# Kernel optimization log

Measured on AMD Instinct MI355X. Metric: run time of the kernel, lower is better.

Reference implementation:

```python
import jax, jax.numpy as jnp
import numpy as np

HEADS = 16  # module init arg `heads`


def setup_inputs() -> dict:
    key = jax.random.key(0)
    k1, k2, k3 = jax.random.split(key, 3)
    B, T, D = 2, 2048, 1024
    x = jax.random.normal(k1, (B, T, D), dtype=jnp.float32)
    w_qkv = jax.random.normal(k2, (D, 3 * D), dtype=jnp.float32) * (1.0 / np.sqrt(D))
    w_proj = jax.random.normal(k3, (D, D), dtype=jnp.float32) * (1.0 / np.sqrt(D))
    b_proj = jnp.zeros((D,), dtype=jnp.float32)
    return {"x": x, "w_qkv": w_qkv, "w_proj": w_proj, "b_proj": b_proj,
            "window": 16, "stride": 16}


def reference(x, w_qkv, w_proj, b_proj, window, stride):
    B, T, D = x.shape
    H = HEADS
    hd = D // H
    scale = 1.0 / np.sqrt(hd)

    qkv = x @ w_qkv                              # [B,T,3D]
    qkv = qkv.reshape(B, T, 3, H, hd)
    q = jnp.transpose(qkv[:, :, 0], (0, 2, 1, 3))  # [B,H,T,hd]
    k = jnp.transpose(qkv[:, :, 1], (0, 2, 1, 3))
    v = jnp.transpose(qkv[:, :, 2], (0, 2, 1, 3))

    # Local window attention: pad front with zeros (matches F.pad), gather
    # sliding windows so patches[..., t, w, :] = k_padded[..., t + w, :].
    pad = window - 1
    k_pad = jnp.pad(k, ((0, 0), (0, 0), (pad, 0), (0, 0)))
    v_pad = jnp.pad(v, ((0, 0), (0, 0), (pad, 0), (0, 0)))
    win_idx = jnp.arange(T)[:, None] + jnp.arange(window)[None, :]  # [T,W]
    pk = k_pad[:, :, win_idx]                    # [B,H,T,W,hd]
    pv = v_pad[:, :, win_idx]                    # [B,H,T,W,hd]

    attn_local = jnp.einsum('bhtd,bhtwd->bhtw', q, pk) * scale
    attn_local = jax.nn.softmax(attn_local, axis=-1)  # zero-pad keys included, as in torch
    out_local = jnp.einsum('bhtw,bhtwd->bhtd', attn_local, pv)

    # Strided global attention
    g_idx = jnp.arange(0, T, stride)
    kg = k[:, :, g_idx]                          # [B,H,G,hd]
    vg = v[:, :, g_idx]
    attn_g = jnp.einsum('bhtd,bhgd->bhtg', q, kg) * scale
    attn_g = jax.nn.softmax(attn_g, axis=-1)
    out_global = jnp.einsum('bhtg,bhgd->bhtd', attn_g, vg)

    out = out_local + out_global                 # [B,H,T,hd]
    out = jnp.transpose(out, (0, 2, 1, 3)).reshape(B, T, D)
    return out @ w_proj + b_proj
```

## Files before the change

### kernel.cpp

```cpp
#include <hip/hip_runtime.h>
#include <hip/hip_bf16.h>

#define BB 2
#define TT 2048
#define DD 1024
#define HH 16
#define HD 64
#define WIN 16
#define NG 128
#define QKVLD 3072

typedef __bf16 bf16x8 __attribute__((ext_vector_type(8)));
typedef _Float16 f16x8 __attribute__((ext_vector_type(8)));
typedef float f32x4 __attribute__((ext_vector_type(4)));
typedef _Float16 h2 __attribute__((ext_vector_type(2)));

__device__ __forceinline__ unsigned short f2bf(float f) {
    union { float f; unsigned int i; } x; x.f = f;
    unsigned int r = x.i + 0x7FFFu + ((x.i >> 16) & 1u);
    return (unsigned short)(r >> 16);
}
__device__ __forceinline__ unsigned short f2h(float f) {
    union { _Float16 h; unsigned short u; } x; x.h = (_Float16)f; return x.u;
}

__device__ __forceinline__ void gll16(const unsigned short* g, unsigned short* l) {
    __builtin_amdgcn_global_load_lds(
        (const __attribute__((address_space(1))) void*)g,
        (__attribute__((address_space(3))) void*)l,
        16, 0, 0);
}

__global__ __launch_bounds__(256) void prepass_kernel(
    const float* __restrict__ x,
    const float* __restrict__ w_qkv,
    const float* __restrict__ w_proj,
    unsigned short* __restrict__ xb,
    unsigned short* __restrict__ wqkvT,
    unsigned short* __restrict__ wprojT)
{
    __shared__ float tile[64][65];
    const int bid = blockIdx.x;
    const int tid = threadIdx.x;

    if (bid < 2048) {
        const size_t i = ((size_t)bid * 256 + tid) * 8;
        float4 f0 = *(const float4*)(x + i);
        float4 f1 = *(const float4*)(x + i + 4);
        ushort4 a = { f2bf(f0.x), f2bf(f0.y), f2bf(f0.z), f2bf(f0.w) };
        ushort4 b = { f2bf(f1.x), f2bf(f1.y), f2bf(f1.z), f2bf(f1.w) };
        *(ushort4*)(xb + i) = a;
        *(ushort4*)(xb + i + 4) = b;
        return;
    }

    const float* w;
    unsigned short* wT;
    int nblk, kblk, N;
    if (bid < 2816) {
        const int b2 = bid - 2048;
        w = w_qkv; wT = wqkvT; N = 3072;
        nblk = b2 % 48; kblk = b2 / 48;
    } else {
        const int b2 = bid - 2816;
        w = w_proj; wT = wprojT; N = 1024;
        nblk = b2 % 16; kblk = b2 / 16;
    }
    const int K = 1024;
    const int n0 = nblk * 64, k0 = kblk * 64;

    {
        const int krow = tid >> 2;
        const int nc0  = (tid & 3) * 16;
        const float* src = w + (size_t)(k0 + krow) * N + n0 + nc0;
        float4 f0 = *(const float4*)(src);
        float4 f1 = *(const float4*)(src + 4);
        float4 f2 = *(const float4*)(src + 8);
        float4 f3 = *(const float4*)(src + 12);
        *(float4*)&tile[krow][nc0]      = f0;
        *(float4*)&tile[krow][nc0 + 4]  = f1;
        *(float4*)&tile[krow][nc0 + 8]  = f2;
        *(float4*)&tile[krow][nc0 + 12] = f3;
    }
    __syncthreads();
    #pragma unroll
    for (int rep = 0; rep < 2; ++rep) {
        const int n   = (tid >> 3) + rep * 32;
        const int kc0 = (tid & 7) * 8;
        union { uint4 v; unsigned short u[8]; } o;
        #pragma unroll
        for (int j = 0; j < 8; ++j) o.u[j] = f2bf(tile[kc0 + j][n]);
        *(uint4*)(wT + (size_t)(n0 + n) * K + k0 + kc0) = o.v;
    }
}

template<int MODE, int TN>
__global__ __launch_bounds__(256) void gemm_kernel(
    const unsigned short* __restrict__ A,
    const unsigned short* __restrict__ Bt,
    void* __restrict__ Cp,
    const float* __restrict__ bias,
    int M, int N, int K)
{
    constexpr int NJ = TN / 32;
    constexpr int BR = TN / 4;
    __shared__ __align__(16) unsigned short As[128 * 32];
    __shared__ __align__(16) unsigned short Bs[TN * 32];
    const int tid  = threadIdx.x;
    const int wave = tid >> 6;
    const int lane = tid & 63;
    const int lm   = lane & 15;
    const int quad = lane >> 4;
    const int wm   = (wave >> 1) * 64;
    const int wn   = (wave & 1) * (TN / 2);
    const int bm   = blockIdx.y * 128;
    const int bn   = blockIdx.x * TN;

    f32x4 acc[4][NJ];
    const f32x4 z4 = { 0.f, 0.f, 0.f, 0.f };
    #pragma unroll
    for (int i = 0; i < 4; ++i)
        #pragma unroll
        for (int j = 0; j < NJ; ++j) acc[i][j] = z4;

    const int lrow = lane >> 2, lcol = (lane & 3) * 8;
    const unsigned short* gA0 = A  + (size_t)(bm + wave * 32 + lrow) * K + lcol;
    const unsigned short* gA1 = gA0 + (size_t)16 * K;
    const unsigned short* gB0 = Bt + (size_t)(bn + wave * BR + lrow) * K + lcol;
    const unsigned short* gB1 = gB0 + (size_t)16 * K;
    unsigned short* lA0 = &As[(wave * 32) * 32];
    unsigned short* lA1 = &As[(wave * 32 + 16) * 32];
    unsigned short* lB0 = &Bs[(wave * BR) * 32];
    unsigned short* lB1 = &Bs[(wave * BR + 16) * 32];

    for (int k0 = 0; k0 < K; k0 += 32) {
        __syncthreads();
        gll16(gA0 + k0, lA0);
        gll16(gA1 + k0, lA1);
        gll16(gB0 + k0, lB0);
        if constexpr (BR == 32) gll16(gB1 + k0, lB1);
        __syncthreads();
        bf16x8 af[4], bfr[NJ];
        #pragma unroll
        for (int i = 0; i < 4; ++i)
            af[i] = *(const bf16x8*)&As[(wm + i * 16 + lm) * 32 + quad * 8];
        #pragma unroll
        for (int j = 0; j < NJ; ++j)
            bfr[j] = *(const bf16x8*)&Bs[(wn + j * 16 + lm) * 32 + quad * 8];
        #pragma unroll
        for (int i = 0; i < 4; ++i)
            #pragma unroll
            for (int j = 0; j < NJ; ++j)
                acc[i][j] = __builtin_amdgcn_mfma_f32_16x16x32_bf16(
                    af[i], bfr[j], acc[i][j], 0, 0, 0);
    }

    #pragma unroll
    for (int i = 0; i < 4; ++i) {
        #pragma unroll
        for (int r = 0; r < 4; ++r) {
            const int row = bm + wm + i * 16 + quad * 4 + r;
            #pragma unroll
            for (int j = 0; j < NJ; ++j) {
                const int col = bn + wn + j * 16 + lm;
                float v = acc[i][j][r];
                if constexpr (MODE == 0) {
                    ((unsigned short*)Cp)[(size_t)row * N + col] = f2h(v);
                } else {
                    ((float*)Cp)[(size_t)row * N + col] = v + bias[col];
                }
            }
        }
    }
}

__global__ __launch_bounds__(256, 3) void attn_kernel(
    const unsigned short* __restrict__ qkv,
    unsigned short* __restrict__ attn_out)
{
    __shared__ __align__(16) unsigned short smem[25728];
    unsigned short* const Kg  = smem;
    unsigned short* const Kl  = smem + 9216;
    unsigned short* const VgT = smem;
    unsigned short* const VlT = smem + 8704;
    unsigned short* const Pb  = smem + 14976;

    const int tid  = threadIdx.x;
    const int wave = tid >> 6;
    const int lane = tid & 63;
    const int lm   = lane & 15;
    const int quad = lane >> 4;
    const int bx   = blockIdx.x;
    const int bh   = bx >> 5;
    const int t0   = (bx & 31) * 64;
    const int b    = bh >> 4;
    const int h    = bh & 15;

    const size_t baseQ = (size_t)(b * TT) * QKVLD + h * HD;

    const int r  = tid >> 1;
    const int hf = tid & 1;
    uint4 vg[4], vl[4];
    {
        const unsigned short* ks = qkv + baseQ + 1024 + (size_t)(16 * r) * QKVLD + hf * 32;
        const unsigned short* vs = ks + 1024;
        unsigned short* kd = Kg + r * 72 + hf * 32;
        #pragma unroll
        for (int j = 0; j < 4; ++j) *(uint4*)(kd + j * 8) = *(const uint4*)(ks + j * 8);
        #pragma unroll
        for (int j = 0; j < 4; ++j) vg[j] = *(const uint4*)(vs + j * 8);

        if (r < 80) {
            const int tl = t0 - 15 + r;
            unsigned short* kld = Kl + r * 72 + hf * 32;
            if (tl < 0 || tl >= TT) {
                const uint4 z = { 0, 0, 0, 0 };
                #pragma unroll
                for (int j = 0; j < 4; ++j) { *(uint4*)(kld + j * 8) = z; vl[j] = z; }
            } else {
                const unsigned short* kls = qkv + baseQ + 1024 + (size_t)tl * QKVLD + hf * 32;
                const unsigned short* vls = kls + 1024;
                #pragma unroll
                for (int j = 0; j < 4; ++j) *(uint4*)(kld + j * 8) = *(const uint4*)(kls + j * 8);
                #pragma unroll
                for (int j = 0; j < 4; ++j) vl[j] = *(const uint4*)(vls + j * 8);
            }
        }
    }

    f16x8 qf[2];
    {
        const unsigned short* qrow = qkv + baseQ + (size_t)(t0 + 16 * wave + lm) * QKVLD;
        const h2 sc = { (_Float16)0.125f, (_Float16)0.125f };
        #pragma unroll
        for (int c = 0; c < 2; ++c) {
            union { uint4 u; h2 hh[4]; f16x8 v; } U;
            U.u = *(const uint4*)(qrow + c * 32 + quad * 8);
            #pragma unroll
            for (int k = 0; k < 4; ++k) U.hh[k] *= sc;
            qf[c] = U.v;
        }
    }

    __syncthreads();

    f32x4 sg[8], sl[2];
    const f32x4 z4 = { 0.f, 0.f, 0.f, 0.f };
    #pragma unroll
    for (int f = 0; f < 8; ++f) sg[f] = z4;
    sl[0] = z4; sl[1] = z4;
    #pragma unroll
    for (int f = 0; f < 8; ++f)
        #pragma unroll
        for (int c = 0; c < 2; ++c)
            sg[f] = __builtin_amdgcn_mfma_f32_16x16x32_f16(
                qf[c], *(const f16x8*)&Kg[(16 * f + lm) * 72 + c * 32 + quad * 8],
                sg[f], 0, 0, 0);
    #pragma unroll
    for (int f = 0; f < 2; ++f)
        #pragma unroll
        for (int c = 0; c < 2; ++c)
            sl[f] = __builtin_amdgcn_mfma_f32_16x16x32_f16(
                qf[c], *(const f16x8*)&Kl[(16 * wave + 16 * f + lm) * 72 + c * 32 + quad * 8],
                sl[f], 0, 0, 0);

    unsigned short* const Pw = Pb + wave * (16 * 168);
    float invg[4], invl[4];
    {
        float dg[4], dl[4];
        #pragma unroll
        for (int rr = 0; rr < 4; ++rr) {
            float s = 0.f;
            #pragma unroll
            for (int f = 0; f < 8; ++f) { float e = __expf(sg[f][rr]); sg[f][rr] = e; s += e; }
            dg[rr] = s;
            const int q = quad * 4 + rr;
            float s2 = 0.f;
            #pragma unroll
            for (int f = 0; f < 2; ++f) {
                const int j2 = 16 * f + lm;
                float e = (j2 >= q && j2 <= q + 15) ? __expf(sl[f][rr]) : 0.f;
                sl[f][rr] = e; s2 += e;
            }
            dl[rr] = s2;
        }
        #pragma unroll
        for (int m = 1; m <= 8; m <<= 1) {
            #pragma unroll
            for (int rr = 0; rr < 4; ++rr) {
                dg[rr] += __shfl_xor(dg[rr], m, 64);
                dl[rr] += __shfl_xor(dl[rr], m, 64);
            }
        }
        #pragma unroll
        for (int rr = 0; rr < 4; ++rr) { invg[rr] = 1.f / dg[rr]; invl[rr] = 1.f / dl[rr]; }
    }

    #pragma unroll
    for (int rr = 0; rr < 4; ++rr) {
        unsigned short* prow = Pw + (quad * 4 + rr) * 168;
        #pragma unroll
        for (int f = 0; f < 8; ++f) prow[16 * f + lm] = f2h(sg[f][rr] * invg[rr]);
        #pragma unroll
        for (int f = 0; f < 2; ++f) prow[128 + 16 * f + lm] = f2h(sl[f][rr] * invl[rr]);
    }

    __syncthreads();

    {
        union { uint4 u[4]; unsigned short s[32]; } Ug;
        #pragma unroll
        for (int j = 0; j < 4; ++j) Ug.u[j] = vg[j];
        #pragma unroll
        for (int j = 0; j < 32; ++j) VgT[(hf * 32 + j) * 136 + r] = Ug.s[j];
        if (r < 80) {
            union { uint4 u[4]; unsigned short s[32]; } Ul;
            #pragma unroll
            for (int j = 0; j < 4; ++j) Ul.u[j] = vl[j];
            #pragma unroll
            for (int j = 0; j < 32; ++j) VlT[(hf * 32 + j) * 88 + r] = Ul.s[j];
        }
    }

    __syncthreads();

    f32x4 o[4];
    #pragma unroll
    for (int c = 0; c < 4; ++c) o[c] = z4;
    #pragma unroll
    for (int kc = 0; kc < 4; ++kc) {
        const f16x8 pa = *(const f16x8*)&Pw[lm * 168 + kc * 32 + quad * 8];
        #pragma unroll
        for (int c = 0; c < 4; ++c)
            o[c] = __builtin_amdgcn_mfma_f32_16x16x32_f16(
                pa, *(const f16x8*)&VgT[(16 * c + lm) * 136 + kc * 32 + quad * 8],
                o[c], 0, 0, 0);
    }
    {
        const f16x8 pa = *(const f16x8*)&Pw[lm * 168 + 128 + quad * 8];
        #pragma unroll
        for (int c = 0; c < 4; ++c)
            o[c] = __builtin_amdgcn_mfma_f32_16x16x32_f16(
                pa, *(const f16x8*)&VlT[(16 * c + lm) * 88 + 16 * wave + quad * 8],
                o[c], 0, 0, 0);
    }

    #pragma unroll
    for (int rr = 0; rr < 4; ++rr) {
        unsigned short* orow_p = Pw + (quad * 4 + rr) * 72;
        #pragma unroll
        for (int c = 0; c < 4; ++c) orow_p[16 * c + lm] = f2bf(o[c][rr]);
    }
    {
        const int orow = lane >> 2;
        const int ocol = (lane & 3) * 16;
        const uint4 d0 = *(const uint4*)&Pw[orow * 72 + ocol];
        const uint4 d1 = *(const uint4*)&Pw[orow * 72 + ocol + 8];
        unsigned short* dst = attn_out + (size_t)(b * TT + t0 + 16 * wave + orow) * DD + h * HD + ocol;
        *(uint4*)(dst)     = d0;
        *(uint4*)(dst + 8) = d1;
    }
}

extern "C" void kernel_launch(void* const* d_in, const int* in_sizes, int n_in,
                              void* d_out, int out_size, void* d_ws, size_t ws_size,
                              hipStream_t stream) {
    const float* x      = (const float*)d_in[0];
    const float* w_qkv  = (const float*)d_in[1];
    const float* w_proj = (const float*)d_in[2];
    const float* b_proj = (const float*)d_in[3];

    char* ws = (char*)d_ws;
    unsigned short* qkv    = (unsigned short*)ws;
    unsigned short* xb     = (unsigned short*)(ws + 25165824);
    unsigned short* attnb  = xb;
    unsigned short* wqkvT  = (unsigned short*)(ws + 25165824 + 8388608);
    unsigned short* wprojT = (unsigned short*)(ws + 25165824 + 8388608 + 6291456);
    float* out = (float*)d_out;

    prepass_kernel<<<3072, 256, 0, stream>>>(x, w_qkv, w_proj, xb, wqkvT, wprojT);

    gemm_kernel<0, 128><<<dim3(3072 / 128, 4096 / 128), 256, 0, stream>>>(
        xb, wqkvT, qkv, nullptr, 4096, 3072, 1024);

    attn_kernel<<<dim3(BB * HH * (TT / 64)), 256, 0, stream>>>(qkv, attnb);

    gemm_kernel<1, 64><<<dim3(1024 / 64, 4096 / 128), 256, 0, stream>>>(
        attnb, wprojT, out, b_proj, 4096, 1024, 1024);
}
```

Before: 158.6 us.

## Keep softmax probabilities in registers via lane shuffles instead of LDS staging

Swaps the MFMA operand order for QK^T so the score tile lands transposed in registers. This lets the probabilities be packed to fp16 with cvt_pkrtz and redistributed into A-fragments with cross-lane shuffles, replacing the per-wave LDS P buffer. Row reductions drop to two shuffles, shared memory shrinks, and launch bounds rise to 4 blocks per CU for more occupancy. The cost is an extra barrier before reusing LDS for the output epilogue, plus more shuffle and select work. Round-to-zero packing also slightly changes rounding versus the previous conversion.

```diff
diff --git a/kernel.cpp b/kernel.cpp
--- a/kernel.cpp
+++ b/kernel.cpp
@@ -14,6 +14,7 @@
 typedef _Float16 f16x8 __attribute__((ext_vector_type(8)));
 typedef float f32x4 __attribute__((ext_vector_type(4)));
 typedef _Float16 h2 __attribute__((ext_vector_type(2)));
+typedef __fp16 pk2_t __attribute__((ext_vector_type(2)));
 
 __device__ __forceinline__ unsigned short f2bf(float f) {
     union { float f; unsigned int i; } x; x.f = f;
@@ -22,6 +23,11 @@
 }
 __device__ __forceinline__ unsigned short f2h(float f) {
     union { _Float16 h; unsigned short u; } x; x.h = (_Float16)f; return x.u;
+}
+__device__ __forceinline__ unsigned int pk2h(float lo, float hi) {
+    union { pk2_t h; unsigned int u; } X;
+    X.h = __builtin_amdgcn_cvt_pkrtz(lo, hi);
+    return X.u;
 }
 
 __device__ __forceinline__ void gll16(const unsigned short* g, unsigned short* l) {
@@ -174,16 +180,41 @@
     }
 }
 
-__global__ __launch_bounds__(256, 3) void attn_kernel(
+__device__ __forceinline__ f16x8 pfrag(unsigned int fa0, unsigned int fa1,
+                                       unsigned int fb0, unsigned int fb1,
+                                       int quad) {
+    const unsigned int t16_0 = (quad == 2) ? fb0 : fa0;
+    const unsigned int t16_1 = (quad == 2) ? fb1 : fa1;
+    const unsigned int t32_0 = (quad == 0) ? fb0 : fa0;
+    const unsigned int t32_1 = (quad == 0) ? fb1 : fa1;
+    const unsigned int t48_0 = (quad == 1) ? fb0 : fa0;
+    const unsigned int t48_1 = (quad == 1) ? fb1 : fa1;
+    const unsigned int s16_0 = (unsigned int)__shfl_xor((int)t16_0, 16, 64);
+    const unsigned int s16_1 = (unsigned int)__shfl_xor((int)t16_1, 16, 64);
+    const unsigned int s32_0 = (unsigned int)__shfl_xor((int)t32_0, 32, 64);
+    const unsigned int s32_1 = (unsigned int)__shfl_xor((int)t32_1, 32, 64);
+    const unsigned int s48_0 = (unsigned int)__shfl_xor((int)t48_0, 48, 64);
+    const unsigned int s48_1 = (unsigned int)__shfl_xor((int)t48_1, 48, 64);
+    unsigned int w0, w1, w2, w3;
+    if (quad == 0)      { w0 = fa0;   w1 = fa1;   w2 = s16_0; w3 = s16_1; }
+    else if (quad == 1) { w0 = s48_0; w1 = s48_1; w2 = s32_0; w3 = s32_1; }
+    else if (quad == 2) { w0 = s32_0; w1 = s32_1; w2 = s48_0; w3 = s48_1; }
+    else                { w0 = s16_0; w1 = s16_1; w2 = fb0;   w3 = fb1;   }
+    union { unsigned int u[4]; f16x8 v; } R;
+    R.u[0] = w0; R.u[1] = w1; R.u[2] = w2; R.u[3] = w3;
+    return R.v;
+}
+
+__global__ __launch_bounds__(256, 4) void attn_kernel(
     const unsigned short* __restrict__ qkv,
     unsigned short* __restrict__ attn_out)
 {
-    __shared__ __align__(16) unsigned short smem[25728];
+    __shared__ __align__(16) unsigned short smem[14976];
     unsigned short* const Kg  = smem;
     unsigned short* const Kl  = smem + 9216;
     unsigned short* const VgT = smem;
     unsigned short* const VlT = smem + 8704;
-    unsigned short* const Pb  = smem + 14976;
+    unsigned short* const Ep  = smem + 9216;
 
     const int tid  = threadIdx.x;
     const int wave = tid >> 6;
@@ -254,55 +285,62 @@
         #pragma unroll
         for (int c = 0; c < 2; ++c)
             sg[f] = __builtin_amdgcn_mfma_f32_16x16x32_f16(
-                qf[c], *(const f16x8*)&Kg[(16 * f + lm) * 72 + c * 32 + quad * 8],
+                *(const f16x8*)&Kg[(16 * f + lm) * 72 + c * 32 + quad * 8], qf[c],
                 sg[f], 0, 0, 0);
     #pragma unroll
     for (int f = 0; f < 2; ++f)
         #pragma unroll
         for (int c = 0; c < 2; ++c)
             sl[f] = __builtin_amdgcn_mfma_f32_16x16x32_f16(
-                qf[c], *(const f16x8*)&Kl[(16 * wave + 16 * f + lm) * 72 + c * 32 + quad * 8],
+                *(const f16x8*)&Kl[(16 * wave + 16 * f + lm) * 72 + c * 32 + quad * 8], qf[c],
                 sl[f], 0, 0, 0);
 
-    unsigned short* const Pw = Pb + wave * (16 * 168);
-    float invg[4], invl[4];
-    {
-        float dg[4], dl[4];
-        #pragma unroll
-        for (int rr = 0; rr < 4; ++rr) {
-            float s = 0.f;
-            #pragma unroll
-            for (int f = 0; f < 8; ++f) { float e = __expf(sg[f][rr]); sg[f][rr] = e; s += e; }
-            dg[rr] = s;
-            const int q = quad * 4 + rr;
-            float s2 = 0.f;
-            #pragma unroll
-            for (int f = 0; f < 2; ++f) {
-                const int j2 = 16 * f + lm;
-                float e = (j2 >= q && j2 <= q + 15) ? __expf(sl[f][rr]) : 0.f;
-                sl[f][rr] = e; s2 += e;
+    float invg, invl;
+    {
+        float dg = 0.f, dl = 0.f;
+        #pragma unroll
+        for (int f = 0; f < 8; ++f)
+            #pragma unroll
+            for (int rr = 0; rr < 4; ++rr) {
+                float e = __expf(sg[f][rr]); sg[f][rr] = e; dg += e;
             }
-            dl[rr] = s2;
-        }
-        #pragma unroll
-        for (int m = 1; m <= 8; m <<= 1) {
+        #pragma unroll
+        for (int f = 0; f < 2; ++f)
             #pragma unroll
             for (int rr = 0; rr < 4; ++rr) {
-                dg[rr] += __shfl_xor(dg[rr], m, 64);
-                dl[rr] += __shfl_xor(dl[rr], m, 64);
+                const int j2 = 16 * f + quad * 4 + rr;
+                const bool in = (j2 >= lm) && (j2 <= lm + 15);
+                float e = in ? __expf(sl[f][rr]) : 0.f;
+                sl[f][rr] = e; dl += e;
             }
-        }
-        #pragma unroll
-        for (int rr = 0; rr < 4; ++rr) { invg[rr] = 1.f / dg[rr]; invl[rr] = 1.f / dl[rr]; }
-    }
-
-    #pragma unroll
-    for (int rr = 0; rr < 4; ++rr) {
-        unsigned short* prow = Pw + (quad * 4 + rr) * 168;
-        #pragma unroll
-        for (int f = 0; f < 8; ++f) prow[16 * f + lm] = f2h(sg[f][rr] * invg[rr]);
-        #pragma unroll
-        for (int f = 0; f < 2; ++f) prow[128 + 16 * f + lm] = f2h(sl[f][rr] * invl[rr]);
+        dg += __shfl_xor(dg, 16, 64);
+        dg += __shfl_xor(dg, 32, 64);
+        dl += __shfl_xor(dl, 16, 64);
+        dl += __shfl_xor(dl, 32, 64);
+        invg = 1.f / dg;
+        invl = 1.f / dl;
+    }
+
+    f16x8 pa0, pa1, pa2, pa3, pal;
+    {
+        #pragma unroll
+        for (int f = 0; f < 8; ++f)
+            #pragma unroll
+            for (int rr = 0; rr < 4; ++rr) sg[f][rr] *= invg;
+        #pragma unroll
+        for (int f = 0; f < 2; ++f)
+            #pragma unroll
+            for (int rr = 0; rr < 4; ++rr) sl[f][rr] *= invl;
+        pa0 = pfrag(pk2h(sg[0][0], sg[0][1]), pk2h(sg[0][2], sg[0][3]),
+                    pk2h(sg[1][0], sg[1][1]), pk2h(sg[1][2], sg[1][3]), quad);
+        pa1 = pfrag(pk2h(sg[2][0], sg[2][1]), pk2h(sg[2][2], sg[2][3]),
+                    pk2h(sg[3][0], sg[3][1]), pk2h(sg[3][2], sg[3][3]), quad);
+        pa2 = pfrag(pk2h(sg[4][0], sg[4][1]), pk2h(sg[4][2], sg[4][3]),
+                    pk2h(sg[5][0], sg[5][1]), pk2h(sg[5][2], sg[5][3]), quad);
+        pa3 = pfrag(pk2h(sg[6][0], sg[6][1]), pk2h(sg[6][2], sg[6][3]),
+                    pk2h(sg[7][0], sg[7][1]), pk2h(sg[7][2], sg[7][3]), quad);
+        pal = pfrag(pk2h(sl[0][0], sl[0][1]), pk2h(sl[0][2], sl[0][3]),
+                    pk2h(sl[1][0], sl[1][1]), pk2h(sl[1][2], sl[1][3]), quad);
     }
 
     __syncthreads();
@@ -328,30 +366,29 @@
     #pragma unroll
     for (int c = 0; c < 4; ++c) o[c] = z4;
     #pragma unroll
-    for (int kc = 0; kc < 4; ++kc) {
-        const f16x8 pa = *(const f16x8*)&Pw[lm * 168 + kc * 32 + quad * 8];
-        #pragma unroll
-        for (int c = 0; c < 4; ++c)
-            o[c] = __builtin_amdgcn_mfma_f32_16x16x32_f16(
-                pa, *(const f16x8*)&VgT[(16 * c + lm) * 136 + kc * 32 + quad * 8],
-                o[c], 0, 0, 0);
-    }
-    {
-        const f16x8 pa = *(const f16x8*)&Pw[lm * 168 + 128 + quad * 8];
-        #pragma unroll
-        for (int c = 0; c < 4; ++c)
-            o[c] = __builtin_amdgcn_mfma_f32_16x16x32_f16(
-                pa, *(const f16x8*)&VlT[(16 * c + lm) * 88 + 16 * wave + quad * 8],
-                o[c], 0, 0, 0);
-    }
-
-    #pragma unroll
-    for (int rr = 0; rr < 4; ++rr) {
-        unsigned short* orow_p = Pw + (quad * 4 + rr) * 72;
-        #pragma unroll
-        for (int c = 0; c < 4; ++c) orow_p[16 * c + lm] = f2bf(o[c][rr]);
-    }
-    {
+    for (int c = 0; c < 4; ++c) {
+        o[c] = __builtin_amdgcn_mfma_f32_16x16x32_f16(
+            pa0, *(const f16x8*)&VgT[(16 * c + lm) * 136 + 0 * 32 + quad * 8], o[c], 0, 0, 0);
+        o[c] = __builtin_amdgcn_mfma_f32_16x16x32_f16(
+            pa1, *(const f16x8*)&VgT[(16 * c + lm) * 136 + 1 * 32 + quad * 8], o[c], 0, 0, 0);
+        o[c] = __builtin_amdgcn_mfma_f32_16x16x32_f16(
+            pa2, *(const f16x8*)&VgT[(16 * c + lm) * 136 + 2 * 32 + quad * 8], o[c], 0, 0, 0);
+        o[c] = __builtin_amdgcn_mfma_f32_16x16x32_f16(
+            pa3, *(const f16x8*)&VgT[(16 * c + lm) * 136 + 3 * 32 + quad * 8], o[c], 0, 0, 0);
+        o[c] = __builtin_amdgcn_mfma_f32_16x16x32_f16(
+            pal, *(const f16x8*)&VlT[(16 * c + lm) * 88 + 16 * wave + quad * 8], o[c], 0, 0, 0);
+    }
+
+    __syncthreads();
+
+    {
+        unsigned short* const Pw = Ep + wave * (16 * 72);
+        #pragma unroll
+        for (int rr = 0; rr < 4; ++rr) {
+            unsigned short* orow_p = Pw + (quad * 4 + rr) * 72;
+            #pragma unroll
+            for (int c = 0; c < 4; ++c) orow_p[16 * c + lm] = f2bf(o[c][rr]);
+        }
         const int orow = lane >> 2;
         const int ocol = (lane & 3) * 16;
         const uint4 d0 = *(const uint4*)&Pw[orow * 72 + ocol];
```

Result: no change. 157.3 us (-0.8%).
